# Optimization experiments

Measured on AMD Instinct MI355X. Metric: run time of the kernel, lower is better.

## Reference

```python
import jax, jax.numpy as jnp
import numpy as np

VOCAB, EMB, FILT, HID, WIN = 32000, 256, 256, 256, 3
B, S = 64, 1024
T = S - WIN + 1  # conv 'valid' output length = 1022


def setup_inputs() -> dict:
    key = jax.random.key(0)
    ks = jax.random.split(key, 12)
    inp = {}
    inp['ipts'] = jax.random.randint(ks[0], (B, S), 0, VOCAB, dtype=jnp.int64 if jax.config.jax_enable_x64 else jnp.int32)
    inp['seq_lengths'] = jax.random.randint(ks[1], (B,), 1, T + 1, dtype=jnp.int32)
    inp['h0'] = jnp.zeros((1, B, HID), jnp.float32)
    inp['c0'] = jnp.zeros((1, B, HID), jnp.float32)
    # learned params
    inp['emb'] = jax.random.normal(ks[2], (VOCAB, EMB), jnp.float32) * 0.1
    inp['emb'] = inp['emb'].at[0].set(0.0)  # padding_idx=0
    inp['conv_w'] = jax.random.normal(ks[3], (WIN, EMB, FILT), jnp.float32) * 0.05  # WIO layout
    inp['conv_b'] = jnp.zeros((FILT,), jnp.float32)
    inp['w_ih'] = jax.random.normal(ks[4], (4 * HID, FILT), jnp.float32) * 0.05  # gate order i,f,g,o
    inp['w_hh'] = jax.random.normal(ks[5], (4 * HID, HID), jnp.float32) * 0.05
    inp['b_ih'] = jnp.zeros((4 * HID,), jnp.float32)
    inp['b_hh'] = jnp.zeros((4 * HID,), jnp.float32)
    inp['lin_w'] = jax.random.normal(ks[6], (1, HID), jnp.float32) * 0.05
    inp['lin_b'] = jnp.zeros((1,), jnp.float32)
    return inp


def reference(ipts, seq_lengths, h0, c0, emb, conv_w, conv_b, w_ih, w_hh, b_ih, b_hh, lin_w, lin_b):
    # Embedding: [B,S,E]
    x = emb[ipts]
    x = jax.lax.conv_general_dilated(x, conv_w, window_strides=(1,), padding='VALID',
                                     dimension_numbers=('NWC', 'WIO', 'NWC')) + conv_b
    # time-major for the RNN: [T,B,F]
    xt = jnp.transpose(x, (1, 0, 2))

    def step(carry, x_t):
        h, c = carry
        g = x_t @ w_ih.T + h @ w_hh.T + (b_ih + b_hh)
        i, f, gg, o = jnp.split(g, 4, axis=-1)
        c = jax.nn.sigmoid(f) * c + jax.nn.sigmoid(i) * jnp.tanh(gg)
        h = jax.nn.sigmoid(o) * jnp.tanh(c)
        return (h, c), h

    _, hs = jax.lax.scan(step, (h0[0], c0[0]), xt)  # hs: [T,B,H]

    # masked mean over real lengths (dropout is identity at eval).
    t = hs.shape[0]
    mask = (jnp.arange(t)[:, None] < seq_lengths[None, :]).astype(hs.dtype)  # [T,B]
    mot = jnp.einsum('tbh,tb->bh', hs, mask) / seq_lengths[:, None].astype(hs.dtype)  # [B,H]

    out = jax.nn.sigmoid(mot @ lin_w.T + lin_b)  # [B,1]
    return out.squeeze(-1)
```

## Files before the change

kernel.cpp:

```cpp
#include <hip/hip_runtime.h>
#include <hip/hip_bf16.h>
#include <math.h>

#define TLEN 1022
#define SLEN 1024
#define NB   64
#define NE   256
#define NF   256
#define NH   256
#define NG   1024
#define TC   128

typedef _Float16 h2_t __attribute__((ext_vector_type(2)));
typedef __attribute__((ext_vector_type(8))) short bf16x8;
typedef __attribute__((ext_vector_type(4))) float f32x4;

#if defined(__has_builtin)
# if __has_builtin(__builtin_amdgcn_sdot4)
#  define HAVE_SDOT4 1
# endif
#endif
#ifndef HAVE_SDOT4
# define HAVE_SDOT4 0
#endif

__device__ __forceinline__ float sigm(float x){ return 1.f/(1.f+__expf(-x)); }
__device__ __forceinline__ float tanh_(float x){ return 1.f - 2.f/(__expf(2.f*x)+1.f); }

__device__ __forceinline__ int sdot4_acc(unsigned int a, unsigned int b, int acc){
#if HAVE_SDOT4
  return __builtin_amdgcn_sdot4((int)a, (int)b, acc, false);
#else
  int s = acc;
  #pragma unroll
  for (int e=0;e<4;++e){
    int av = (int)(signed char)((a >> (8*e)) & 0xff);
    int bv = (int)(signed char)((b >> (8*e)) & 0xff);
    s += av*bv;
  }
  return s;
#endif
}
__device__ __forceinline__ unsigned short f2bf(float x){
  __hip_bfloat16 b = __float2bfloat16(x);
  return __builtin_bit_cast(unsigned short, b);
}

__global__ __launch_bounds__(256) void k_bias(const float* __restrict__ conv_b,
                                              const float* __restrict__ w_ih,
                                              const float* __restrict__ b_ih,
                                              const float* __restrict__ b_hh,
                                              float* __restrict__ bias4){
  int g = blockIdx.x*256 + threadIdx.x;
  const float* row = w_ih + (size_t)g*NF;
  float s = b_ih[g] + b_hh[g];
  for (int f=0; f<NF; f+=4){
    float4 w4 = *(const float4*)(row+f);
    float4 c4 = *(const float4*)(conv_b+f);
    s += w4.x*c4.x + w4.y*c4.y + w4.z*c4.z + w4.w*c4.w;
  }
  bias4[g] = s;
}

__global__ __launch_bounds__(256) void k_scale(const float* __restrict__ w_hh,
                                               float* __restrict__ stepv,
                                               float* __restrict__ sws){
  int row = blockIdx.x*256 + threadIdx.x;
  const float* p = w_hh + (size_t)row*NH;
  float m = 0.f;
  for (int c=0;c<NH;c+=4){
    float4 v = *(const float4*)(p+c);
    m = fmaxf(m, fmaxf(fmaxf(fabsf(v.x),fabsf(v.y)), fmaxf(fabsf(v.z),fabsf(v.w))));
  }
  float st = fmaxf(m, 1e-20f) / 127.f;
  stepv[row] = st;
  sws[row]   = st / 127.f;
}

__global__ __launch_bounds__(256) void k_pack6(const float* __restrict__ w_hh,
                                               const float* __restrict__ stepv,
                                               uint4* __restrict__ pq6){
  int gid = blockIdx.x*256 + threadIdx.x;
  int i = gid >> 10, tid = gid & 1023;
  int w = tid >> 6, l = tid & 63, kq = w >> 2, jq = w & 3;
  unsigned int words[4];
  #pragma unroll
  for (int r=0; r<4; ++r){
    int row = jq*256 + l*4 + r;
    float st = stepv[row];
    unsigned int acc = 0;
    #pragma unroll
    for (int e=0; e<4; ++e){
      int col = kq*64 + i*4 + e;
      int q = __float2int_rn(w_hh[(size_t)row*NH + col] / st);
      q = max(-127, min(127, q));
      acc |= ((unsigned int)(unsigned char)(signed char)q) << (8*e);
    }
    words[r] = acc;
  }
  pq6[(size_t)i*1024 + tid] = make_uint4(words[0],words[1],words[2],words[3]);
}

__global__ __launch_bounds__(256) void k_cw2(const float* __restrict__ w_ih,
                                             const float* __restrict__ conv_w,
                                             unsigned short* __restrict__ cw2t){
  __shared__ float al[64][17];
  __shared__ float bl[16][64];
  const int n0  = blockIdx.x*64;
  const int m0  = blockIdx.y*64;
  const int tid = threadIdx.x;
  const int ty  = tid>>4, tx = tid&15;
  const int rr  = tid>>2, kq = (tid&3)<<2;
  float acc[4][4];
  #pragma unroll
  for (int i=0;i<4;++i){ acc[i][0]=0.f; acc[i][1]=0.f; acc[i][2]=0.f; acc[i][3]=0.f; }

  for (int k0=0; k0<256; k0+=16){
    __syncthreads();
    {
      float4 v = *(const float4*)(w_ih + (size_t)(m0+rr)*NF + k0 + kq);
      al[rr][kq+0]=v.x; al[rr][kq+1]=v.y; al[rr][kq+2]=v.z; al[rr][kq+3]=v.w;
      float4 u = *(const float4*)(conv_w + (size_t)(n0+rr)*NF + k0 + kq);
      bl[kq+0][rr]=u.x; bl[kq+1][rr]=u.y; bl[kq+2][rr]=u.z; bl[kq+3][rr]=u.w;
    }
    __syncthreads();
    #pragma unroll
    for (int kk=0; kk<16; ++kk){
      float a0=al[ty*4+0][kk], a1=al[ty*4+1][kk], a2=al[ty*4+2][kk], a3=al[ty*4+3][kk];
      float4 bv = *(const float4*)&bl[kk][tx*4];
      acc[0][0]+=a0*bv.x; acc[0][1]+=a0*bv.y; acc[0][2]+=a0*bv.z; acc[0][3]+=a0*bv.w;
      acc[1][0]+=a1*bv.x; acc[1][1]+=a1*bv.y; acc[1][2]+=a1*bv.z; acc[1][3]+=a1*bv.w;
      acc[2][0]+=a2*bv.x; acc[2][1]+=a2*bv.y; acc[2][2]+=a2*bv.z; acc[2][3]+=a2*bv.w;
      acc[3][0]+=a3*bv.x; acc[3][1]+=a3*bv.y; acc[3][2]+=a3*bv.z; acc[3][3]+=a3*bv.w;
    }
  }
  #pragma unroll
  for (int i=0;i<4;++i){
    size_t r = (size_t)m0 + ty*4 + i;
    unsigned int p0 = (unsigned int)f2bf(acc[i][0]) | ((unsigned int)f2bf(acc[i][1])<<16);
    unsigned int p1 = (unsigned int)f2bf(acc[i][2]) | ((unsigned int)f2bf(acc[i][3])<<16);
    *(uint2*)(cw2t + r*768 + n0 + tx*4) = make_uint2(p0, p1);
  }
}

__global__ __attribute__((amdgpu_flat_work_group_size(1024,1024)))
__attribute__((amdgpu_waves_per_eu(4,4)))
void k_step(const int* __restrict__ ipts, const float* __restrict__ emb,
            const unsigned short* __restrict__ cw2t, const float* __restrict__ bias4,
            const unsigned short* __restrict__ xh_r, unsigned short* __restrict__ xh_w,
            const uint4* __restrict__ pq6, const float* __restrict__ sws,
            const float* __restrict__ h0, const float* __restrict__ c0,
            const int* __restrict__ seqlen,
            const float* __restrict__ lin_w, const float* __restrict__ lin_b,
            float* __restrict__ h_ws, float* __restrict__ c_ws, float* __restrict__ ms_ws,
            float* __restrict__ out,
            int t0r, int tcount, int is_first, int is_last,
            int t0f, int do_rnn, int n_fxg){
  __shared__ __align__(16) char smem[115968];
  const int tid  = threadIdx.x;
  const int nrnn = do_rnn ? 64 : 0;

  if ((int)blockIdx.x < nrnn){
    uint4*        wlds = (uint4*)smem;
    float*        part = (float*)(smem + 98304);
    unsigned int* hq   = (unsigned int*)(smem + 114688);
    float*        red  = (float*)(smem + 114944);
    const int b  = blockIdx.x;
    const int l  = tid & 63, w = tid >> 6;
    const int kq = w >> 2, jq = w & 3;
    const int rbase = jq*256 + l*4;

    #pragma unroll
    for (int i=0;i<6;++i) wlds[i*1024 + tid] = pq6[(size_t)i*1024 + tid];

    uint4 wreg[10];
    #pragma unroll
    for (int i=6;i<16;++i) wreg[i-6] = pq6[(size_t)i*1024 + tid];
    #pragma unroll
    for (int i=0;i<10;++i)
      asm volatile("" : "+v"(wreg[i].x), "+v"(wreg[i].y), "+v"(wreg[i].z), "+v"(wreg[i].w));

    float swr[4];
    #pragma unroll
    for (int r=0;r<4;++r) swr[r] = sws[rbase + r];

    const int L = seqlen[b];
    float creg = 0.f, msum = 0.f, hlast = 0.f;
    if (tid < 256){
      float hv;
      if (is_first){ hv = h0[(size_t)b*NH + tid]; creg = c0[(size_t)b*NH + tid]; }
      else { hv = h_ws[b*256 + tid]; creg = c_ws[b*256 + tid]; msum = ms_ws[b*256 + tid]; }
      hlast = hv;
      int q = __float2int_rn(hv * 127.f); q = max(-127, min(127, q));
      ((signed char*)hq)[tid] = (signed char)q;
    }
    __syncthreads();

    const unsigned short* xrow = xh_r + (size_t)b*NG + tid;

    for (int tl=0; tl<tcount; ++tl){
      unsigned short xr0=0, xr1=0, xr2=0, xr3=0;
      if (tid < 256){
        const unsigned short* xr = xrow + (size_t)tl*NB*NG;
        xr0 = xr[0]; xr1 = xr[256]; xr2 = xr[512]; xr3 = xr[768];
      }

      unsigned int hws[16];
      #pragma unroll
      for (int c=0;c<4;++c){
        uint4 t = *(const uint4*)&hq[kq*16 + c*4];
        hws[c*4+0]=t.x; hws[c*4+1]=t.y; hws[c*4+2]=t.z; hws[c*4+3]=t.w;
      }

      int pa[4] = {0,0,0,0};
      #pragma unroll
      for (int i=0;i<16;++i){
        unsigned int hw = hws[i];
        uint4 wv4 = (i < 6) ? wlds[i*1024 + tid] : wreg[i-6];
        pa[0] = sdot4_acc(wv4.x, hw, pa[0]);
        pa[1] = sdot4_acc(wv4.y, hw, pa[1]);
        pa[2] = sdot4_acc(wv4.z, hw, pa[2]);
        pa[3] = sdot4_acc(wv4.w, hw, pa[3]);
      }
      *(float4*)&part[kq*1024 + rbase] = make_float4(
          (float)pa[0]*swr[0], (float)pa[1]*swr[1],
          (float)pa[2]*swr[2], (float)pa[3]*swr[3]);
      __syncthreads();

      if (tid < 256){
        unsigned short xr4[4] = {xr0, xr1, xr2, xr3};
        float a[4];
        #pragma unroll
        for (int g=0; g<4; ++g){
          float s = (float)__builtin_bit_cast(_Float16, xr4[g]);
          int idx = g*256 + tid;
          #pragma unroll
          for (int k=0;k<4;++k) s += part[k*1024 + idx];
          a[g] = s;
        }
        float si = sigm(a[0]), sf = sigm(a[1]), so = sigm(a[3]);
        float tg = tanh_(a[2]);
        creg = sf*creg + si*tg;
        float h2 = so*tanh_(creg);
        if (t0r + tl < L) msum += h2;
        hlast = h2;
        int q2 = __float2int_rn(h2 * 127.f); q2 = max(-127, min(127, q2));
        ((signed char*)hq)[tid] = (signed char)q2;
      }
      __syncthreads();
    }

    if (tid < 256){
      h_ws[b*256 + tid]  = hlast;
      c_ws[b*256 + tid]  = creg;
      ms_ws[b*256 + tid] = msum;
    }

    if (is_last){
      if (tid < 256) red[tid] = (msum / (float)L) * lin_w[tid];
      __syncthreads();
      if (tid < 64){
        float s = red[tid] + red[tid+64] + red[tid+128] + red[tid+192];
        #pragma unroll
        for (int off=32; off>0; off>>=1) s += __shfl_down(s, off);
        if (tid==0) out[b] = sigm(s + lin_b[0]);
      }
    }
  } else {
    int fidx = (int)blockIdx.x - nrnn;
    if (fidx >= n_fxg) return;
    unsigned short* A_l  = (unsigned short*)smem;
    unsigned short* B_l  = (unsigned short*)(smem + 18432);
    int*            tokl = (int*)(smem + 55296);
    const int l  = tid & 63, wv = tid >> 6;
    const int m0 = (fidx >> 2) * 128;
    const int n0 = (fidx & 3) * 256;
    const int TL0 = m0 >> 6;

    if (tid < 256){
      int tv = tid >> 6, bb = tid & 63;
      int s = t0f + TL0 + tv;
      tokl[tid] = (s < SLEN) ? ipts[bb*SLEN + s] : 0;
    }

    f32x4 acc[2][4];
    #pragma unroll
    for (int mt=0; mt<2; ++mt)
      #pragma unroll
      for (int nt=0; nt<4; ++nt)
        acc[mt][nt] = (f32x4){0.f,0.f,0.f,0.f};

    const int wm = wv >> 2, wn = wv & 3;
    const int lr = l & 15, lk = l >> 4;

    for (int ks = 0; ks < 12; ++ks){
      const int w0 = ks >> 2;
      const int e0 = (ks & 3) << 6;
      __syncthreads();
      {
        int row = tid >> 3, off = tid & 7;
        int tok = tokl[((row>>6) + w0)*64 + (row & 63)];
        const float* src = emb + (size_t)tok*NE + e0 + off*8;
        float4 f0 = *(const float4*)src;
        float4 f1 = *(const float4*)(src+4);
        unsigned int p0 = (unsigned int)f2bf(f0.x) | ((unsigned int)f2bf(f0.y)<<16);
        unsigned int p1 = (unsigned int)f2bf(f0.z) | ((unsigned int)f2bf(f0.w)<<16);
        unsigned int p2 = (unsigned int)f2bf(f1.x) | ((unsigned int)f2bf(f1.y)<<16);
        unsigned int p3 = (unsigned int)f2bf(f1.z) | ((unsigned int)f2bf(f1.w)<<16);
        *(uint4*)&A_l[row*72 + off*8] = make_uint4(p0,p1,p2,p3);
      }
      #pragma unroll
      for (int s2 = 0; s2 < 2; ++s2){
        int seg = tid + s2*1024;
        int row = seg >> 3, off = seg & 7;
        uint4 v = *(const uint4*)(cw2t + (size_t)(n0+row)*768 + (ks<<6) + off*8);
        *(uint4*)&B_l[row*72 + off*8] = v;
      }
      __syncthreads();
      #pragma unroll
      for (int kf = 0; kf < 2; ++kf){
        bf16x8 af[2], bfr[4];
        #pragma unroll
        for (int mt=0; mt<2; ++mt)
          af[mt] = *(const bf16x8*)&A_l[(wm*32 + mt*16 + lr)*72 + kf*32 + lk*8];
        #pragma unroll
        for (int nt=0; nt<4; ++nt)
          bfr[nt] = *(const bf16x8*)&B_l[(wn*64 + nt*16 + lr)*72 + kf*32 + lk*8];
        #pragma unroll
        for (int mt=0; mt<2; ++mt)
          #pragma unroll
          for (int nt=0; nt<4; ++nt)
            acc[mt][nt] = __builtin_amdgcn_mfma_f32_16x16x32_bf16(af[mt], bfr[nt], acc[mt][nt], 0,0,0);
      }
    }

    float bia[4];
    #pragma unroll
    for (int nt=0; nt<4; ++nt) bia[nt] = bias4[n0 + wn*64 + nt*16 + lr];
    #pragma unroll
    for (int mt=0; mt<2; ++mt){
      #pragma unroll
      for (int nt=0; nt<4; ++nt){
        #pragma unroll
        for (int r=0; r<4; ++r){
          int row = m0 + wm*32 + mt*16 + lk*4 + r;
          int col = n0 + wn*64 + nt*16 + lr;
          _Float16 hv = (_Float16)(acc[mt][nt][r] + bia[nt]);
          xh_w[(size_t)row*NG + col] = __builtin_bit_cast(unsigned short, hv);
        }
      }
    }
  }
}

extern "C" void kernel_launch(void* const* d_in, const int* in_sizes, int n_in,
                              void* d_out, int out_size, void* d_ws, size_t ws_size,
                              hipStream_t stream){
  const int*   ipts   = (const int*)d_in[0];
  const int*   seqlen = (const int*)d_in[1];
  const float* h0     = (const float*)d_in[2];
  const float* c0     = (const float*)d_in[3];
  const float* emb    = (const float*)d_in[4];
  const float* conv_w = (const float*)d_in[5];
  const float* conv_b = (const float*)d_in[6];
  const float* w_ih   = (const float*)d_in[7];
  const float* w_hh   = (const float*)d_in[8];
  const float* b_ih   = (const float*)d_in[9];
  const float* b_hh   = (const float*)d_in[10];
  const float* lin_w  = (const float*)d_in[11];
  const float* lin_b  = (const float*)d_in[12];
  float* out = (float*)d_out;

  char* ws = (char*)d_ws;
  const size_t XH_B   = (size_t)TC*NB*NG*2;
  const size_t CW2_B  = (size_t)NG*768*2;
  const size_t PQ_B   = (size_t)16*1024*16;
  size_t off = 0;
  unsigned short* xhA   = (unsigned short*)(ws + off); off += XH_B;
  unsigned short* xhB   = (unsigned short*)(ws + off); off += XH_B;
  unsigned short* cw2t  = (unsigned short*)(ws + off); off += CW2_B;
  uint4*          pq6   = (uint4*)(ws + off);          off += PQ_B;
  float*          stepv = (float*)(ws + off);          off += 4096;
  float*          sws   = (float*)(ws + off);          off += 4096;
  float*          bias4 = (float*)(ws + off);          off += 4096;
  float*          h_ws  = (float*)(ws + off);          off += 65536;
  float*          c_ws  = (float*)(ws + off);          off += 65536;
  float*          ms_ws = (float*)(ws + off);          off += 65536;

  k_bias <<<dim3(4),      dim3(256), 0, stream>>>(conv_b, w_ih, b_ih, b_hh, bias4);
  k_scale<<<dim3(4),      dim3(256), 0, stream>>>(w_hh, stepv, sws);
  k_pack6<<<dim3(64),     dim3(256), 0, stream>>>(w_hh, stepv, pq6);
  k_cw2  <<<dim3(12, 16), dim3(256), 0, stream>>>(w_ih, conv_w, cw2t);

  unsigned short* bufs[2] = {xhA, xhB};
  const int nchunks = (TLEN + TC - 1) / TC;
  auto nf_of = [](int tc){ return 4 * ((tc + 1) / 2); };

  {
    int tc0 = (TLEN < TC) ? TLEN : TC;
    int nf0 = nf_of(tc0);
    k_step<<<dim3(nf0), dim3(1024), 0, stream>>>(
        ipts, emb, cw2t, bias4, bufs[0], bufs[0], pq6, sws, h0, c0, seqlen,
        lin_w, lin_b, h_ws, c_ws, ms_ws, out,
        0, 0, 0, 0, 0, 0, nf0);
  }

  for (int c = 0; c < nchunks; ++c){
    int t0 = c*TC;
    int tcount = (TLEN - t0 < TC) ? (TLEN - t0) : TC;
    int nf = 0, t0f = 0;
    unsigned short* xw = bufs[0];
    if (c + 1 < nchunks){
      int t0n = (c+1)*TC;
      int tcn = (TLEN - t0n < TC) ? (TLEN - t0n) : TC;
      nf  = nf_of(tcn);
      t0f = t0n;
      xw  = bufs[(c+1) & 1];
    }
    k_step<<<dim3(64 + nf), dim3(1024), 0, stream>>>(
        ipts, emb, cw2t, bias4, bufs[c & 1], xw, pq6, sws, h0, c0, seqlen,
        lin_w, lin_b, h_ws, c_ws, ms_ws, out,
        t0, tcount, (c==0), (c==nchunks-1), t0f, 1, nf);
  }
}
```

Measured before the change: 1.206 ms.

## Reduce LSTM gate partials via wave shuffles and compute gate activations in all threads

Re-packs the quantized recurrent weights so the four K-quarter partial sums for each gate row sit in lanes of the same wavefront. They are then reduced with cross-lane shuffles instead of a shared-memory partial buffer. Each thread also loads its own input-projection values and applies the sigmoid/tanh activation in parallel across all 1024 threads, so only the cell update stays on 256 threads. This shortens the serial per-timestep critical path and shrinks LDS, at the cost of extra shuffle instructions and redundant activation work in the kq lanes.

```diff
diff --git a/kernel.cpp b/kernel.cpp
--- a/kernel.cpp
+++ b/kernel.cpp
@@ -77,16 +77,17 @@
   sws[row]   = st / 127.f;
 }
 
-__global__ __launch_bounds__(256) void k_pack6(const float* __restrict__ w_hh,
+__global__ __launch_bounds__(256) void k_pack7(const float* __restrict__ w_hh,
                                                const float* __restrict__ stepv,
-                                               uint4* __restrict__ pq6){
+                                               uint4* __restrict__ pq7){
   int gid = blockIdx.x*256 + threadIdx.x;
   int i = gid >> 10, tid = gid & 1023;
-  int w = tid >> 6, l = tid & 63, kq = w >> 2, jq = w & 3;
+  int w = tid >> 6, l = tid & 63;
+  int gb = w & 3, ub = w >> 2, ul = l & 15, kq = l >> 4;
   unsigned int words[4];
   #pragma unroll
   for (int r=0; r<4; ++r){
-    int row = jq*256 + l*4 + r;
+    int row = gb*256 + ub*64 + ul*4 + r;
     float st = stepv[row];
     unsigned int acc = 0;
     #pragma unroll
@@ -98,7 +99,7 @@
     }
     words[r] = acc;
   }
-  pq6[(size_t)i*1024 + tid] = make_uint4(words[0],words[1],words[2],words[3]);
+  pq7[(size_t)i*1024 + tid] = make_uint4(words[0],words[1],words[2],words[3]);
 }
 
 __global__ __launch_bounds__(256) void k_cw2(const float* __restrict__ w_ih,
@@ -148,7 +149,7 @@
 void k_step(const int* __restrict__ ipts, const float* __restrict__ emb,
             const unsigned short* __restrict__ cw2t, const float* __restrict__ bias4,
             const unsigned short* __restrict__ xh_r, unsigned short* __restrict__ xh_w,
-            const uint4* __restrict__ pq6, const float* __restrict__ sws,
+            const uint4* __restrict__ pq7, const float* __restrict__ sws,
             const float* __restrict__ h0, const float* __restrict__ c0,
             const int* __restrict__ seqlen,
             const float* __restrict__ lin_w, const float* __restrict__ lin_b,
@@ -156,26 +157,28 @@
             float* __restrict__ out,
             int t0r, int tcount, int is_first, int is_last,
             int t0f, int do_rnn, int n_fxg){
-  __shared__ __align__(16) char smem[115968];
+  __shared__ __align__(16) char smem[103936];
   const int tid  = threadIdx.x;
   const int nrnn = do_rnn ? 64 : 0;
 
   if ((int)blockIdx.x < nrnn){
     uint4*        wlds = (uint4*)smem;
-    float*        part = (float*)(smem + 98304);
-    unsigned int* hq   = (unsigned int*)(smem + 114688);
-    float*        red  = (float*)(smem + 114944);
+    float*        actl = (float*)(smem + 98304);
+    unsigned int* hq   = (unsigned int*)(smem + 102400);
+    float*        red  = (float*)(smem + 102656);
     const int b  = blockIdx.x;
     const int l  = tid & 63, w = tid >> 6;
-    const int kq = w >> 2, jq = w & 3;
-    const int rbase = jq*256 + l*4;
-
-    #pragma unroll
-    for (int i=0;i<6;++i) wlds[i*1024 + tid] = pq6[(size_t)i*1024 + tid];
+    const int gb = w & 3, ub = w >> 2;
+    const int ul = l & 15, kq = l >> 4;
+    const int ubase = ub*64 + ul*4;
+    const int rbase = gb*256 + ubase;
+
+    #pragma unroll
+    for (int i=0;i<6;++i) wlds[i*1024 + tid] = pq7[(size_t)i*1024 + tid];
 
     uint4 wreg[10];
     #pragma unroll
-    for (int i=6;i<16;++i) wreg[i-6] = pq6[(size_t)i*1024 + tid];
+    for (int i=6;i<16;++i) wreg[i-6] = pq7[(size_t)i*1024 + tid];
     #pragma unroll
     for (int i=0;i<10;++i)
       asm volatile("" : "+v"(wreg[i].x), "+v"(wreg[i].y), "+v"(wreg[i].z), "+v"(wreg[i].w));
@@ -196,14 +199,11 @@
     }
     __syncthreads();
 
-    const unsigned short* xrow = xh_r + (size_t)b*NG + tid;
+    const unsigned short* xrow = xh_r + (size_t)b*NG + rbase;
 
     for (int tl=0; tl<tcount; ++tl){
-      unsigned short xr0=0, xr1=0, xr2=0, xr3=0;
-      if (tid < 256){
-        const unsigned short* xr = xrow + (size_t)tl*NB*NG;
-        xr0 = xr[0]; xr1 = xr[256]; xr2 = xr[512]; xr3 = xr[768];
-      }
+      uint2 xw = *(const uint2*)(xrow + (size_t)tl*NB*NG);
+      const unsigned short* xs = (const unsigned short*)&xw;
 
       unsigned int hws[16];
       #pragma unroll
@@ -222,26 +222,24 @@
         pa[2] = sdot4_acc(wv4.z, hw, pa[2]);
         pa[3] = sdot4_acc(wv4.w, hw, pa[3]);
       }
-      *(float4*)&part[kq*1024 + rbase] = make_float4(
-          (float)pa[0]*swr[0], (float)pa[1]*swr[1],
-          (float)pa[2]*swr[2], (float)pa[3]*swr[3]);
+
+      float av[4];
+      #pragma unroll
+      for (int r=0;r<4;++r){
+        int p = pa[r];
+        p += __shfl_xor(p, 16, 64);
+        p += __shfl_xor(p, 32, 64);
+        float a = (float)p * swr[r] + (float)__builtin_bit_cast(_Float16, xs[r]);
+        av[r] = (gb == 2) ? tanh_(a) : sigm(a);
+      }
+      if (kq == 0)
+        *(float4*)&actl[rbase] = make_float4(av[0],av[1],av[2],av[3]);
       __syncthreads();
 
       if (tid < 256){
-        unsigned short xr4[4] = {xr0, xr1, xr2, xr3};
-        float a[4];
-        #pragma unroll
-        for (int g=0; g<4; ++g){
-          float s = (float)__builtin_bit_cast(_Float16, xr4[g]);
-          int idx = g*256 + tid;
-          #pragma unroll
-          for (int k=0;k<4;++k) s += part[k*1024 + idx];
-          a[g] = s;
-        }
-        float si = sigm(a[0]), sf = sigm(a[1]), so = sigm(a[3]);
-        float tg = tanh_(a[2]);
-        creg = sf*creg + si*tg;
-        float h2 = so*tanh_(creg);
+        float ai = actl[tid], af = actl[256+tid], ag = actl[512+tid], ao = actl[768+tid];
+        creg = af*creg + ai*ag;
+        float h2 = ao*tanh_(creg);
         if (t0r + tl < L) msum += h2;
         hlast = h2;
         int q2 = __float2int_rn(h2 * 127.f); q2 = max(-127, min(127, q2));
@@ -379,7 +377,7 @@
   unsigned short* xhA   = (unsigned short*)(ws + off); off += XH_B;
   unsigned short* xhB   = (unsigned short*)(ws + off); off += XH_B;
   unsigned short* cw2t  = (unsigned short*)(ws + off); off += CW2_B;
-  uint4*          pq6   = (uint4*)(ws + off);          off += PQ_B;
+  uint4*          pq7   = (uint4*)(ws + off);          off += PQ_B;
   float*          stepv = (float*)(ws + off);          off += 4096;
   float*          sws   = (float*)(ws + off);          off += 4096;
   float*          bias4 = (float*)(ws + off);          off += 4096;
@@ -389,7 +387,7 @@
 
   k_bias <<<dim3(4),      dim3(256), 0, stream>>>(conv_b, w_ih, b_ih, b_hh, bias4);
   k_scale<<<dim3(4),      dim3(256), 0, stream>>>(w_hh, stepv, sws);
-  k_pack6<<<dim3(64),     dim3(256), 0, stream>>>(w_hh, stepv, pq6);
+  k_pack7<<<dim3(64),     dim3(256), 0, stream>>>(w_hh, stepv, pq7);
   k_cw2  <<<dim3(12, 16), dim3(256), 0, stream>>>(w_ih, conv_w, cw2t);
 
   unsigned short* bufs[2] = {xhA, xhB};
@@ -400,7 +398,7 @@
     int tc0 = (TLEN < TC) ? TLEN : TC;
     int nf0 = nf_of(tc0);
     k_step<<<dim3(nf0), dim3(1024), 0, stream>>>(
-        ipts, emb, cw2t, bias4, bufs[0], bufs[0], pq6, sws, h0, c0, seqlen,
+        ipts, emb, cw2t, bias4, bufs[0], bufs[0], pq7, sws, h0, c0, seqlen,
         lin_w, lin_b, h_ws, c_ws, ms_ws, out,
         0, 0, 0, 0, 0, 0, nf0);
   }
@@ -418,7 +416,7 @@
       xw  = bufs[(c+1) & 1];
     }
     k_step<<<dim3(64 + nf), dim3(1024), 0, stream>>>(
-        ipts, emb, cw2t, bias4, bufs[c & 1], xw, pq6, sws, h0, c0, seqlen,
+        ipts, emb, cw2t, bias4, bufs[c & 1], xw, pq7, sws, h0, c0, seqlen,
         lin_w, lin_b, h_ws, c_ws, ms_ws, out,
         t0, tcount, (c==0), (c==nchunks-1), t0f, 1, nf);
   }
```

Result: slower. 1.834 ms (+52.1%).

## Process two batch rows per RNN block to reuse recurrent weights

Applied to the files above, without the earlier changes.

Each persistent RNN block now handles two batch sequences instead of one, so every int8 weight load from LDS/registers feeds two sdot4 accumulations. The RNN grid halves from 64 to 32 blocks and the LDS partial-sum buffer doubles. This leaves more CUs for the overlapped input-projection GEMM blocks and amortizes weight fetches. The cost is more per-block compute on the serial recurrence path and a larger shared-memory footprint.

```diff
diff --git a/kernel.cpp b/kernel.cpp
--- a/kernel.cpp
+++ b/kernel.cpp
@@ -156,19 +156,21 @@
             float* __restrict__ out,
             int t0r, int tcount, int is_first, int is_last,
             int t0f, int do_rnn, int n_fxg){
-  __shared__ __align__(16) char smem[115968];
+  __shared__ __align__(16) char smem[133632];
   const int tid  = threadIdx.x;
-  const int nrnn = do_rnn ? 64 : 0;
+  const int nrnn = do_rnn ? 32 : 0;
 
   if ((int)blockIdx.x < nrnn){
     uint4*        wlds = (uint4*)smem;
     float*        part = (float*)(smem + 98304);
-    unsigned int* hq   = (unsigned int*)(smem + 114688);
-    float*        red  = (float*)(smem + 114944);
-    const int b  = blockIdx.x;
+    unsigned int* hq   = (unsigned int*)(smem + 131072);
+    float*        red  = (float*)(smem + 131584);
+    const int b0 = blockIdx.x * 2;
     const int l  = tid & 63, w = tid >> 6;
     const int kq = w >> 2, jq = w & 3;
     const int rbase = jq*256 + l*4;
+    const int bsel  = tid >> 8;
+    const int uu    = tid & 255;
 
     #pragma unroll
     for (int i=0;i<6;++i) wlds[i*1024 + tid] = pq6[(size_t)i*1024 + tid];
@@ -184,58 +186,66 @@
     #pragma unroll
     for (int r=0;r<4;++r) swr[r] = sws[rbase + r];
 
-    const int L = seqlen[b];
+    int L = 0;
     float creg = 0.f, msum = 0.f, hlast = 0.f;
-    if (tid < 256){
+    if (tid < 512){
+      const int b = b0 + bsel;
+      L = seqlen[b];
       float hv;
-      if (is_first){ hv = h0[(size_t)b*NH + tid]; creg = c0[(size_t)b*NH + tid]; }
-      else { hv = h_ws[b*256 + tid]; creg = c_ws[b*256 + tid]; msum = ms_ws[b*256 + tid]; }
+      if (is_first){ hv = h0[(size_t)b*NH + uu]; creg = c0[(size_t)b*NH + uu]; }
+      else { hv = h_ws[b*256 + uu]; creg = c_ws[b*256 + uu]; msum = ms_ws[b*256 + uu]; }
       hlast = hv;
       int q = __float2int_rn(hv * 127.f); q = max(-127, min(127, q));
-      ((signed char*)hq)[tid] = (signed char)q;
+      ((signed char*)hq)[bsel*256 + uu] = (signed char)q;
     }
     __syncthreads();
 
-    const unsigned short* xrow = xh_r + (size_t)b*NG + tid;
+    const unsigned short* xrow = xh_r + (size_t)(b0 + bsel)*NG + uu;
 
     for (int tl=0; tl<tcount; ++tl){
       unsigned short xr0=0, xr1=0, xr2=0, xr3=0;
-      if (tid < 256){
+      if (tid < 512){
         const unsigned short* xr = xrow + (size_t)tl*NB*NG;
         xr0 = xr[0]; xr1 = xr[256]; xr2 = xr[512]; xr3 = xr[768];
       }
 
-      unsigned int hws[16];
+      unsigned int h0w[16], h1w[16];
       #pragma unroll
       for (int c=0;c<4;++c){
-        uint4 t = *(const uint4*)&hq[kq*16 + c*4];
-        hws[c*4+0]=t.x; hws[c*4+1]=t.y; hws[c*4+2]=t.z; hws[c*4+3]=t.w;
-      }
-
-      int pa[4] = {0,0,0,0};
+        uint4 t0_ = *(const uint4*)&hq[0*64 + kq*16 + c*4];
+        uint4 t1_ = *(const uint4*)&hq[1*64 + kq*16 + c*4];
+        h0w[c*4+0]=t0_.x; h0w[c*4+1]=t0_.y; h0w[c*4+2]=t0_.z; h0w[c*4+3]=t0_.w;
+        h1w[c*4+0]=t1_.x; h1w[c*4+1]=t1_.y; h1w[c*4+2]=t1_.z; h1w[c*4+3]=t1_.w;
+      }
+
+      int pa0[4] = {0,0,0,0}, pa1[4] = {0,0,0,0};
       #pragma unroll
       for (int i=0;i<16;++i){
-        unsigned int hw = hws[i];
         uint4 wv4 = (i < 6) ? wlds[i*1024 + tid] : wreg[i-6];
-        pa[0] = sdot4_acc(wv4.x, hw, pa[0]);
-        pa[1] = sdot4_acc(wv4.y, hw, pa[1]);
-        pa[2] = sdot4_acc(wv4.z, hw, pa[2]);
-        pa[3] = sdot4_acc(wv4.w, hw, pa[3]);
-      }
-      *(float4*)&part[kq*1024 + rbase] = make_float4(
-          (float)pa[0]*swr[0], (float)pa[1]*swr[1],
-          (float)pa[2]*swr[2], (float)pa[3]*swr[3]);
+        unsigned int a0 = h0w[i], a1 = h1w[i];
+        pa0[0] = sdot4_acc(wv4.x, a0, pa0[0]);  pa1[0] = sdot4_acc(wv4.x, a1, pa1[0]);
+        pa0[1] = sdot4_acc(wv4.y, a0, pa0[1]);  pa1[1] = sdot4_acc(wv4.y, a1, pa1[1]);
+        pa0[2] = sdot4_acc(wv4.z, a0, pa0[2]);  pa1[2] = sdot4_acc(wv4.z, a1, pa1[2]);
+        pa0[3] = sdot4_acc(wv4.w, a0, pa0[3]);  pa1[3] = sdot4_acc(wv4.w, a1, pa1[3]);
+      }
+      *(float4*)&part[0*4096 + kq*1024 + rbase] = make_float4(
+          (float)pa0[0]*swr[0], (float)pa0[1]*swr[1],
+          (float)pa0[2]*swr[2], (float)pa0[3]*swr[3]);
+      *(float4*)&part[1*4096 + kq*1024 + rbase] = make_float4(
+          (float)pa1[0]*swr[0], (float)pa1[1]*swr[1],
+          (float)pa1[2]*swr[2], (float)pa1[3]*swr[3]);
       __syncthreads();
 
-      if (tid < 256){
+      if (tid < 512){
         unsigned short xr4[4] = {xr0, xr1, xr2, xr3};
+        const float* pb = part + bsel*4096;
         float a[4];
         #pragma unroll
         for (int g=0; g<4; ++g){
           float s = (float)__builtin_bit_cast(_Float16, xr4[g]);
-          int idx = g*256 + tid;
+          int idx = g*256 + uu;
           #pragma unroll
-          for (int k=0;k<4;++k) s += part[k*1024 + idx];
+          for (int k=0;k<4;++k) s += pb[k*1024 + idx];
           a[g] = s;
         }
         float si = sigm(a[0]), sf = sigm(a[1]), so = sigm(a[3]);
@@ -245,25 +255,28 @@
         if (t0r + tl < L) msum += h2;
         hlast = h2;
         int q2 = __float2int_rn(h2 * 127.f); q2 = max(-127, min(127, q2));
-        ((signed char*)hq)[tid] = (signed char)q2;
+        ((signed char*)hq)[bsel*256 + uu] = (signed char)q2;
       }
       __syncthreads();
     }
 
-    if (tid < 256){
-      h_ws[b*256 + tid]  = hlast;
-      c_ws[b*256 + tid]  = creg;
-      ms_ws[b*256 + tid] = msum;
+    if (tid < 512){
+      const int b = b0 + bsel;
+      h_ws[b*256 + uu]  = hlast;
+      c_ws[b*256 + uu]  = creg;
+      ms_ws[b*256 + uu] = msum;
     }
 
     if (is_last){
-      if (tid < 256) red[tid] = (msum / (float)L) * lin_w[tid];
+      if (tid < 512) red[bsel*256 + uu] = (msum / (float)L) * lin_w[uu];
       __syncthreads();
-      if (tid < 64){
-        float s = red[tid] + red[tid+64] + red[tid+128] + red[tid+192];
+      if (tid < 128){
+        int bs = tid >> 6, ln = tid & 63;
+        float s = red[bs*256 + ln] + red[bs*256 + ln + 64]
+                + red[bs*256 + ln + 128] + red[bs*256 + ln + 192];
         #pragma unroll
         for (int off=32; off>0; off>>=1) s += __shfl_down(s, off);
-        if (tid==0) out[b] = sigm(s + lin_b[0]);
+        if (ln==0) out[b0 + bs] = sigm(s + lin_b[0]);
       }
     }
   } else {
@@ -417,7 +430,7 @@
       t0f = t0n;
       xw  = bufs[(c+1) & 1];
     }
-    k_step<<<dim3(64 + nf), dim3(1024), 0, stream>>>(
+    k_step<<<dim3(32 + nf), dim3(1024), 0, stream>>>(
         ipts, emb, cw2t, bias4, bufs[c & 1], xw, pq6, sws, h0, c0, seqlen,
         lin_w, lin_b, h_ws, c_ws, ms_ws, out,
         t0, tcount, (c==0), (c==nchunks-1), t0f, 1, nf);
```

Measured after the change: 1.924 ms. 1.6x slower.
